# Kernel optimization log

Hardware: AMD Instinct MI355X
Metric: run time of the kernel (lower is better)

Reference implementation:

```python
import jax, jax.numpy as jnp
import numpy as np

N_NODES = 50000
N_EDGES = 800000
IN_C, HID_C, OUT_C = 128, 128, 64
BN_EPS = 1e-5


def _normalized_adj(edge_index, N):
    # Mirrors remove_self_loops + add_self_loops + symmetric GCN normalization.
    src, dst = edge_index[0], edge_index[1]
    mask = (src != dst).astype(jnp.float32)  # drop original self loops
    # degree of dst over (masked edges + added self loops)
    deg = jax.ops.segment_sum(mask, dst, num_segments=N) + 1.0
    dinv = jnp.where(deg > 0, deg ** -0.5, 0.0)
    w = mask * dinv[src] * dinv[dst]          # weights for original edges
    w_self = dinv * dinv                      # weights for added self loops
    return src, dst, w, w_self


def _spmm(src, dst, w, w_self, x):
    # torch.sparse.mm(adj, x): out[i] = sum_{e: src[e]=i} w[e] * x[dst[e]] + w_self[i]*x[i]
    agg = jax.ops.segment_sum(w[:, None] * x[dst], src, num_segments=x.shape[0])
    return agg + w_self[:, None] * x


def setup_inputs() -> dict:
    key = jax.random.key(0)
    ks = jax.random.split(key, 4)
    x = jax.random.normal(ks[0], (N_NODES, IN_C), dtype=jnp.float32)
    edge_index = jax.random.randint(ks[1], (2, N_EDGES), 0, N_NODES, dtype=jnp.int64)
    # glorot init for GCN linear weights
    s1 = np.sqrt(6.0 / (IN_C + HID_C)).astype(np.float32)
    s2 = np.sqrt(6.0 / (HID_C + OUT_C)).astype(np.float32)
    W1 = jax.random.uniform(ks[2], (IN_C, HID_C), jnp.float32, -s1, s1)
    W2 = jax.random.uniform(ks[3], (HID_C, OUT_C), jnp.float32, -s2, s2)
    return {
        "x": x,
        "edge_index": edge_index,
        "W1": W1,
        "b1": jnp.zeros((HID_C,), jnp.float32),
        "gamma": jnp.ones((HID_C,), jnp.float32),
        "beta": jnp.zeros((HID_C,), jnp.float32),
        "W2": W2,
        "b2": jnp.zeros((OUT_C,), jnp.float32),
    }


def reference(x, edge_index, W1, b1, gamma, beta, W2, b2):
    N = x.shape[0]
    src, dst, w, w_self = _normalized_adj(edge_index, N)
    # layer 1: linear -> SpMM -> BN (batch stats) -> ReLU (dropout: eval)
    h = x @ W1 + b1
    h = _spmm(src, dst, w, w_self, h)
    mean = h.mean(axis=0)
    var = jnp.mean((h - mean) ** 2, axis=0)
    h = (h - mean) * jax.lax.rsqrt(var + BN_EPS) * gamma + beta
    h = jax.nn.relu(h)
    # layer 2: linear -> SpMM
    h = h @ W2 + b2
    h = _spmm(src, dst, w, w_self, h)
    return h
```

## Files before the change

### kernel.cpp

```cpp
#include <hip/hip_runtime.h>

#define N_NODES 50000
#define N_EDGES 800000
#define BN_EPS 1e-5f
#define NPAD 50176
#define SCAN_BLOCKS 98

#define S_SLICES 64
#define R_RANGES 4
#define BINS 16384
#define NP4 (R_RANGES * BINS)
#define ES (N_EDGES / S_SLICES)

#define XS_STRIDE 68

typedef unsigned int uint;
typedef unsigned short ushort;
typedef float floatx4 __attribute__((ext_vector_type(4)));
typedef short bf16x8 __attribute__((ext_vector_type(8)));

__device__ __forceinline__ float bfl(uint u) { return __uint_as_float(u << 16); }
__device__ __forceinline__ float bfh(uint u) { return __uint_as_float(u & 0xffff0000u); }
__device__ __forceinline__ uint pack_bf2(float a, float b) {
    uint ua = __float_as_uint(a), ub = __float_as_uint(b);
    ua += 0x7fffu + ((ua >> 16) & 1u);
    ub += 0x7fffu + ((ub >> 16) & 1u);
    return (ua >> 16) | (ub & 0xffff0000u);
}
__device__ __forceinline__ ushort bf1(float x) {
    uint u = __float_as_uint(x);
    u += 0x7fffu + ((u >> 16) & 1u);
    return (ushort)(u >> 16);
}
__device__ __forceinline__ void acc8(float* a, uint4 h, float w) {
    a[0] += w * bfl(h.x); a[1] += w * bfh(h.x);
    a[2] += w * bfl(h.y); a[3] += w * bfh(h.y);
    a[4] += w * bfl(h.z); a[5] += w * bfh(h.z);
    a[6] += w * bfl(h.w); a[7] += w * bfh(h.w);
}

__global__ __launch_bounds__(256) void prep_w_kernel(const float* __restrict__ W1,
                                                     const float* __restrict__ W2,
                                                     uint* __restrict__ W1t,
                                                     uint* __restrict__ W2t) {
    int t = blockIdx.x * 256 + threadIdx.x;
    if (t < 8192) {
        int n = t >> 6, kk = t & 63;
        W1t[t] = pack_bf2(W1[(2 * kk) * 128 + n], W1[(2 * kk + 1) * 128 + n]);
    } else if (t < 12288) {
        int u = t - 8192;
        int n = u >> 6, kk = u & 63;
        W2t[u] = pack_bf2(W2[(2 * kk) * 64 + n], W2[(2 * kk + 1) * 64 + n]);
    }
}

__global__ __launch_bounds__(256) void count_hist_kernel(const int* __restrict__ src,
                                                         const int* __restrict__ dst,
                                                         ushort* __restrict__ part_cnt,
                                                         ushort* __restrict__ part_deg) {
    __shared__ uint cnt_lds[BINS / 2];
    __shared__ uint deg_lds[BINS / 2];
    const int s = blockIdx.x / R_RANGES;
    const int r = blockIdx.x % R_RANGES;
    const int base = r * BINS;
    for (int j = threadIdx.x; j < BINS / 2; j += 256) { cnt_lds[j] = 0u; deg_lds[j] = 0u; }
    __syncthreads();
    const int4* s4 = (const int4*)(src + s * ES);
    const int4* d4 = (const int4*)(dst + s * ES);
#pragma unroll 2
    for (int g = threadIdx.x; g < ES / 4; g += 256) {
        int4 sv = s4[g];
        int4 dv = d4[g];
#pragma unroll
        for (int k = 0; k < 4; ++k) {
            int ss = (&sv.x)[k], dd = (&dv.x)[k];
            if (ss != dd) {
                int a = ss - base;
                if ((unsigned)a < (unsigned)BINS)
                    atomicAdd(&cnt_lds[a >> 1], 1u << ((a & 1) * 16));
                int b = dd - base;
                if ((unsigned)b < (unsigned)BINS)
                    atomicAdd(&deg_lds[b >> 1], 1u << ((b & 1) * 16));
            }
        }
    }
    __syncthreads();
    uint* pc = (uint*)&part_cnt[s * NP4 + base];
    uint* pd = (uint*)&part_deg[s * NP4 + base];
    for (int j = threadIdx.x; j < BINS / 2; j += 256) { pc[j] = cnt_lds[j]; pd[j] = deg_lds[j]; }
}

__global__ __launch_bounds__(256) void dinv_rowcnt_kernel(const ushort* __restrict__ part_deg,
                                                          const ushort* __restrict__ part_cnt,
                                                          float* __restrict__ dinv,
                                                          int* __restrict__ rowcnt) {
    int i = (blockIdx.x * 256 + threadIdx.x) * 2;
    uint dg0 = 0, dg1 = 0, rc0 = 0, rc1 = 0;
#pragma unroll 8
    for (int s = 0; s < S_SLICES; ++s) {
        uint vd = *(const uint*)&part_deg[s * NP4 + i];
        uint vc = *(const uint*)&part_cnt[s * NP4 + i];
        dg0 += vd & 0xffffu; dg1 += vd >> 16;
        rc0 += vc & 0xffffu; rc1 += vc >> 16;
    }
    *(int2*)&rowcnt[i] = make_int2((int)rc0, (int)rc1);
    if (i < N_NODES) dinv[i] = rsqrtf((float)dg0 + 1.0f);
    if (i + 1 < N_NODES) dinv[i + 1] = rsqrtf((float)dg1 + 1.0f);
}

__global__ __launch_bounds__(512) void scan1_kernel(const int* __restrict__ rowcnt,
                                                    int* __restrict__ rowptr,
                                                    int* __restrict__ psum) {
    __shared__ int buf[512];
    int t = threadIdx.x;
    int g = blockIdx.x * 512 + t;
    buf[t] = rowcnt[g];
    __syncthreads();
#pragma unroll
    for (int off = 1; off < 512; off <<= 1) {
        int x = (t >= off) ? buf[t - off] : 0;
        __syncthreads();
        buf[t] += x;
        __syncthreads();
    }
    rowptr[g] = buf[t];
    if (t == 511) psum[blockIdx.x] = buf[511];
}

__global__ void scan2_kernel(int* __restrict__ psum) {
    if (threadIdx.x == 0) {
        int acc = 0;
        for (int i = 0; i < SCAN_BLOCKS; ++i) {
            int v = psum[i];
            psum[i] = acc;
            acc += v;
        }
    }
}

__global__ __launch_bounds__(256) void cursor_init_kernel(const int* __restrict__ rowcnt,
                                                          int* __restrict__ rowptr,
                                                          const int* __restrict__ psum,
                                                          const ushort* __restrict__ part_cnt,
                                                          int* __restrict__ cursor) {
    int i = (blockIdx.x * 256 + threadIdx.x) * 2;
    int ps = psum[i >> 9];
    int b0 = rowptr[i] - rowcnt[i] + ps;
    int b1 = rowptr[i + 1] - rowcnt[i + 1] + ps;
    *(int2*)&rowptr[i] = make_int2(b0, b1);
#pragma unroll 8
    for (int s = 0; s < S_SLICES; ++s) {
        *(int2*)&cursor[s * NP4 + i] = make_int2(b0, b1);
        uint vc = *(const uint*)&part_cnt[s * NP4 + i];
        b0 += (int)(vc & 0xffffu);
        b1 += (int)(vc >> 16);
    }
}

__global__ __launch_bounds__(256) void fill_lds_kernel(const int* __restrict__ src,
                                                       const int* __restrict__ dst,
                                                       const float* __restrict__ dinv,
                                                       const int* __restrict__ cursor,
                                                       int2* __restrict__ epair) {
    __shared__ int curs[BINS];
    const int s = blockIdx.x / R_RANGES;
    const int r = blockIdx.x % R_RANGES;
    const int base = r * BINS;
    const int* gc = &cursor[s * NP4 + base];
    for (int j = threadIdx.x; j < BINS; j += 256) curs[j] = gc[j];
    __syncthreads();
    const int4* s4 = (const int4*)(src + s * ES);
    const int4* d4 = (const int4*)(dst + s * ES);
#pragma unroll 2
    for (int g = threadIdx.x; g < ES / 4; g += 256) {
        int4 sv = s4[g];
        int4 dv = d4[g];
#pragma unroll
        for (int k = 0; k < 4; ++k) {
            int ss = (&sv.x)[k], dd = (&dv.x)[k];
            int a = ss - base;
            if (ss != dd && (unsigned)a < (unsigned)BINS) {
                int pos = atomicAdd(&curs[a], 1);
                epair[pos] = make_int2(dd, __float_as_int(dinv[ss] * dinv[dd]));
            }
        }
    }
}

__global__ __launch_bounds__(256) void gemm1_mfma_kernel(const float* __restrict__ X,
                                                         const uint* __restrict__ W1t,
                                                         const float* __restrict__ bias,
                                                         ushort* __restrict__ Hbf) {
    __shared__ uint lds[(64 + 128) * XS_STRIDE];
    uint* Xs = lds;
    uint* Ws = lds + 64 * XS_STRIDE;
    const int t = threadIdx.x;
    const int rowBase = blockIdx.x * 64;

    {
        int r = t >> 2, q = t & 3;
        int arow = rowBase + r;
        uint* xd = &Xs[r * XS_STRIDE + q * 16];
        if (arow < N_NODES) {
            const float4* xp = (const float4*)&X[arow * 128 + q * 32];
#pragma unroll
            for (int i = 0; i < 8; ++i) {
                float4 v = xp[i];
                xd[2 * i]     = pack_bf2(v.x, v.y);
                xd[2 * i + 1] = pack_bf2(v.z, v.w);
            }
        } else {
#pragma unroll
            for (int i = 0; i < 16; ++i) xd[i] = 0u;
        }
    }
    {
        int n = t >> 1, half = t & 1;
        const uint4* wp = (const uint4*)&W1t[n * 64 + half * 32];
        uint* wd = &Ws[n * XS_STRIDE + half * 32];
#pragma unroll
        for (int i = 0; i < 8; ++i) *(uint4*)&wd[i * 4] = wp[i];
    }
    __syncthreads();

    const int wv = t >> 6, lane = t & 63;
    const int lr = lane & 15;
    const int ko = (lane >> 4) * 4;
    const int m0 = wv * 16;
    floatx4 acc[8];
#pragma unroll
    for (int j = 0; j < 8; ++j) acc[j] = (floatx4){0.f, 0.f, 0.f, 0.f};

#pragma unroll
    for (int ks = 0; ks < 4; ++ks) {
        const int kb = ks * 16 + ko;
        bf16x8 a = *(bf16x8*)&Xs[(m0 + lr) * XS_STRIDE + kb];
#pragma unroll
        for (int j = 0; j < 8; ++j) {
            bf16x8 b = *(bf16x8*)&Ws[(j * 16 + lr) * XS_STRIDE + kb];
            acc[j] = __builtin_amdgcn_mfma_f32_16x16x32_bf16(a, b, acc[j], 0, 0, 0);
        }
    }
    const int rbase = rowBase + m0 + (lane >> 4) * 4;
#pragma unroll
    for (int j = 0; j < 8; ++j) {
        const int col = j * 16 + lr;
        const float bb = bias[col];
#pragma unroll
        for (int r = 0; r < 4; ++r) {
            int row = rbase + r;
            if (row < N_NODES) Hbf[row * 128 + col] = bf1(acc[j][r] + bb);
        }
    }
}

__global__ __launch_bounds__(256) void gemm2_mfma_kernel(const uint* __restrict__ Hin,
                                                         const uint* __restrict__ W2t,
                                                         const float* __restrict__ bias,
                                                         const float* __restrict__ scale,
                                                         const float* __restrict__ shift,
                                                         ushort* __restrict__ Hbf) {
    __shared__ uint lds[(64 + 64) * XS_STRIDE];
    uint* Xs = lds;
    uint* Ws = lds + 64 * XS_STRIDE;
    const int t = threadIdx.x;
    const int rowBase = blockIdx.x * 64;

    {
        int r = t >> 2, q = t & 3;
        int arow = rowBase + r;
        uint* xd = &Xs[r * XS_STRIDE + q * 16];
        if (arow < N_NODES) {
            const uint* hp = &Hin[arow * 64 + q * 16];
#pragma unroll
            for (int i = 0; i < 16; ++i) {
                uint u = hp[i];
                int m = q * 16 + i;
                float2 sc = *(const float2*)&scale[2 * m];
                float2 sh = *(const float2*)&shift[2 * m];
                float a0 = fmaxf(0.f, bfl(u) * sc.x + sh.x);
                float a1 = fmaxf(0.f, bfh(u) * sc.y + sh.y);
                xd[i] = pack_bf2(a0, a1);
            }
        } else {
#pragma unroll
            for (int i = 0; i < 16; ++i) xd[i] = 0u;
        }
    }
    if (t < 128) {
        int n = t >> 1, half = t & 1;
        const uint4* wp = (const uint4*)&W2t[n * 64 + half * 32];
        uint* wd = &Ws[n * XS_STRIDE + half * 32];
#pragma unroll
        for (int i = 0; i < 8; ++i) *(uint4*)&wd[i * 4] = wp[i];
    }
    __syncthreads();

    const int wv = t >> 6, lane = t & 63;
    const int lr = lane & 15;
    const int ko = (lane >> 4) * 4;
    const int m0 = wv * 16;
    floatx4 acc[4];
#pragma unroll
    for (int j = 0; j < 4; ++j) acc[j] = (floatx4){0.f, 0.f, 0.f, 0.f};

#pragma unroll
    for (int ks = 0; ks < 4; ++ks) {
        const int kb = ks * 16 + ko;
        bf16x8 a = *(bf16x8*)&Xs[(m0 + lr) * XS_STRIDE + kb];
#pragma unroll
        for (int j = 0; j < 4; ++j) {
            bf16x8 b = *(bf16x8*)&Ws[(j * 16 + lr) * XS_STRIDE + kb];
            acc[j] = __builtin_amdgcn_mfma_f32_16x16x32_bf16(a, b, acc[j], 0, 0, 0);
        }
    }
    const int rbase = rowBase + m0 + (lane >> 4) * 4;
#pragma unroll
    for (int j = 0; j < 4; ++j) {
        const int col = j * 16 + lr;
        const float bb = bias[col];
#pragma unroll
        for (int r = 0; r < 4; ++r) {
            int row = rbase + r;
            if (row < N_NODES) Hbf[row * 64 + col] = bf1(acc[j][r] + bb);
        }
    }
}

template <int C, bool OUT_BF16>
__global__ __launch_bounds__(256) void spmm_bf16_kernel(const int* __restrict__ rowptr,
                                                        const int2* __restrict__ epair,
                                                        const float* __restrict__ dinv,
                                                        const uint* __restrict__ H,
                                                        void* __restrict__ outv) {
    constexpr int LPR = C / 8;
    constexpr int RPB = 256 / LPR;
    constexpr int US  = C / 2;
    const int t = threadIdx.x;
    const int lane = t % LPR;
    const int row = blockIdx.x * RPB + t / LPR;
    if (row >= N_NODES) return;
    const int cu = lane * 4;
    const float di = dinv[row];

    float acc[8];
    {
        uint4 hv = *(const uint4*)&H[row * US + cu];
        float w = di * di;
        acc[0] = w * bfl(hv.x); acc[1] = w * bfh(hv.x);
        acc[2] = w * bfl(hv.y); acc[3] = w * bfh(hv.y);
        acc[4] = w * bfl(hv.z); acc[5] = w * bfh(hv.z);
        acc[6] = w * bfl(hv.w); acc[7] = w * bfh(hv.w);
    }
    const int e0 = rowptr[row], e1 = rowptr[row + 1];
    int e = e0;
    if ((e & 1) && e < e1) {
        int2 p = epair[e];
        uint4 h = *(const uint4*)&H[p.x * US + cu];
        acc8(acc, h, __int_as_float(p.y));
        ++e;
    }
    const int4* ep4 = (const int4*)epair;
    for (; e + 8 <= e1; e += 8) {
        int4 qa = ep4[(e >> 1) + 0];
        int4 qb = ep4[(e >> 1) + 1];
        int4 qc = ep4[(e >> 1) + 2];
        int4 qd = ep4[(e >> 1) + 3];
        uint4 h0 = *(const uint4*)&H[qa.x * US + cu];
        uint4 h1 = *(const uint4*)&H[qa.z * US + cu];
        uint4 h2 = *(const uint4*)&H[qb.x * US + cu];
        uint4 h3 = *(const uint4*)&H[qb.z * US + cu];
        uint4 h4 = *(const uint4*)&H[qc.x * US + cu];
        uint4 h5 = *(const uint4*)&H[qc.z * US + cu];
        uint4 h6 = *(const uint4*)&H[qd.x * US + cu];
        uint4 h7 = *(const uint4*)&H[qd.z * US + cu];
        acc8(acc, h0, __int_as_float(qa.y));
        acc8(acc, h1, __int_as_float(qa.w));
        acc8(acc, h2, __int_as_float(qb.y));
        acc8(acc, h3, __int_as_float(qb.w));
        acc8(acc, h4, __int_as_float(qc.y));
        acc8(acc, h5, __int_as_float(qc.w));
        acc8(acc, h6, __int_as_float(qd.y));
        acc8(acc, h7, __int_as_float(qd.w));
    }
    for (; e + 2 <= e1; e += 2) {
        int4 q = ep4[e >> 1];
        uint4 h0 = *(const uint4*)&H[q.x * US + cu];
        uint4 h1 = *(const uint4*)&H[q.z * US + cu];
        acc8(acc, h0, __int_as_float(q.y));
        acc8(acc, h1, __int_as_float(q.w));
    }
    if (e < e1) {
        int2 p = epair[e];
        uint4 h = *(const uint4*)&H[p.x * US + cu];
        acc8(acc, h, __int_as_float(p.y));
    }
    if (OUT_BF16) {
        uint4 o;
        o.x = pack_bf2(acc[0], acc[1]);
        o.y = pack_bf2(acc[2], acc[3]);
        o.z = pack_bf2(acc[4], acc[5]);
        o.w = pack_bf2(acc[6], acc[7]);
        *(uint4*)&((uint*)outv)[row * US + cu] = o;
    } else {
        float* out = (float*)outv;
        *(float4*)&out[row * C + lane * 8]     = make_float4(acc[0], acc[1], acc[2], acc[3]);
        *(float4*)&out[row * C + lane * 8 + 4] = make_float4(acc[4], acc[5], acc[6], acc[7]);
    }
}

__global__ __launch_bounds__(256) void bn_stats_kernel(const uint* __restrict__ H,
                                                       float* __restrict__ sum,
                                                       float* __restrict__ sumsq) {
    int uc = threadIdx.x & 63;
    int quarter = threadIdx.x >> 6;
    float s0 = 0.f, q0 = 0.f, s1 = 0.f, q1 = 0.f;
    for (int r = blockIdx.x * 4 + quarter; r < N_NODES; r += 512) {
        uint u = H[r * 64 + uc];
        float a = bfl(u), b = bfh(u);
        s0 += a; q0 += a * a;
        s1 += b; q1 += b * b;
    }
    __shared__ float red[4][256];
    red[0][threadIdx.x] = s0; red[1][threadIdx.x] = q0;
    red[2][threadIdx.x] = s1; red[3][threadIdx.x] = q1;
    __syncthreads();
    if (quarter == 0) {
        float ts0 = 0.f, tq0 = 0.f, ts1 = 0.f, tq1 = 0.f;
#pragma unroll
        for (int k = 0; k < 4; ++k) {
            ts0 += red[0][k * 64 + uc]; tq0 += red[1][k * 64 + uc];
            ts1 += red[2][k * 64 + uc]; tq1 += red[3][k * 64 + uc];
        }
        atomicAdd(&sum[2 * uc], ts0);
        atomicAdd(&sum[2 * uc + 1], ts1);
        atomicAdd(&sumsq[2 * uc], tq0);
        atomicAdd(&sumsq[2 * uc + 1], tq1);
    }
}

__global__ void bn_finalize_kernel(const float* __restrict__ sum,
                                   const float* __restrict__ sumsq,
                                   const float* __restrict__ gamma,
                                   const float* __restrict__ beta,
                                   float* __restrict__ scale,
                                   float* __restrict__ shift) {
    int c = threadIdx.x;
    if (c < 128) {
        float mean = sum[c] * (1.0f / N_NODES);
        float var = sumsq[c] * (1.0f / N_NODES) - mean * mean;
        float sc = gamma[c] * rsqrtf(var + BN_EPS);
        scale[c] = sc;
        shift[c] = beta[c] - mean * sc;
    }
}

extern "C" void kernel_launch(void* const* d_in, const int* in_sizes, int n_in,
                              void* d_out, int out_size, void* d_ws, size_t ws_size,
                              hipStream_t stream) {
    const float* x     = (const float*)d_in[0];
    const int*   ei    = (const int*)d_in[1];
    const float* W1    = (const float*)d_in[2];
    const float* b1    = (const float*)d_in[3];
    const float* gamma = (const float*)d_in[4];
    const float* beta  = (const float*)d_in[5];
    const float* W2    = (const float*)d_in[6];
    const float* b2    = (const float*)d_in[7];
    float* out = (float*)d_out;
    const int* src = ei;
    const int* dst = ei + N_EDGES;

    float* ws     = (float*)d_ws;
    float* dinv   = ws;
    float* stats  = ws + NPAD;
    int*   psum   = (int*)(ws + NPAD + 512);
    int*   rowcnt = psum + 128;
    int*   rowptr = rowcnt + NPAD;
    float* big    = (float*)(rowptr + NPAD);
    int2*   epair    = (int2*)big;
    ushort* part_cnt = (ushort*)(big + 1600000);
    ushort* part_deg = (ushort*)(big + 3700000);
    int*    cursor   = (int*)(big + 5800000);
    ushort* h1bf     = (ushort*)(big + 1600000);
    uint*   h1agg    = (uint*)(big + 4800000);
    ushort* h2bf     = h1bf;
    uint*   W1t      = (uint*)(big + 10000000);
    uint*   W2t      = W1t + 8192;
    float* sum    = stats;
    float* sumsq  = stats + 128;
    float* scale  = stats + 256;
    float* shift  = stats + 384;

    hipMemsetAsync(stats, 0, 512 * sizeof(float), stream);

    prep_w_kernel<<<48, 256, 0, stream>>>(W1, W2, W1t, W2t);

    count_hist_kernel<<<S_SLICES * R_RANGES, 256, 0, stream>>>(src, dst, part_cnt, part_deg);
    dinv_rowcnt_kernel<<<NPAD / 512, 256, 0, stream>>>(part_deg, part_cnt, dinv, rowcnt);

    scan1_kernel<<<SCAN_BLOCKS, 512, 0, stream>>>(rowcnt, rowptr, psum);
    scan2_kernel<<<1, 64, 0, stream>>>(psum);
    cursor_init_kernel<<<NPAD / 512, 256, 0, stream>>>(rowcnt, rowptr, psum, part_cnt, cursor);
    fill_lds_kernel<<<S_SLICES * R_RANGES, 256, 0, stream>>>(src, dst, dinv, cursor, epair);

    gemm1_mfma_kernel<<<(N_NODES + 63) / 64, 256, 0, stream>>>(x, W1t, b1, h1bf);

    spmm_bf16_kernel<128, true><<<(N_NODES + 15) / 16, 256, 0, stream>>>(
        rowptr, epair, dinv, (const uint*)h1bf, (void*)h1agg);

    bn_stats_kernel<<<128, 256, 0, stream>>>(h1agg, sum, sumsq);
    bn_finalize_kernel<<<1, 128, 0, stream>>>(sum, sumsq, gamma, beta, scale, shift);

    gemm2_mfma_kernel<<<(N_NODES + 63) / 64, 256, 0, stream>>>(h1agg, W2t, b2, scale, shift, h2bf);

    spmm_bf16_kernel<64, false><<<(N_NODES + 31) / 32, 256, 0, stream>>>(
        rowptr, epair, dinv, (const uint*)h2bf, (void*)out);
}
```

Measured before the change: 256.7 us.

## Fuse degree reduction with block scan and fold BN finalize into gemm2

Merges the degree/rowcount reduction with the per-block prefix scan, and moves the cross-block psum accumulation into cursor_init. The separate scan1, scan2 and bn_finalize launches and the memset go away. Stats zeroing now happens in the first block of the reduce kernel, and every gemm2 block computes BN scale and shift into shared memory. This removes several tiny serial launches and their gaps. In exchange it adds redundant per-block work in gemm2, a serial psum loop in thread 0 of each cursor_init block, and uses LDS-strided scale reads.

```diff
diff --git a/kernel.cpp b/kernel.cpp
--- a/kernel.cpp
+++ b/kernel.cpp
@@ -90,11 +90,16 @@
     for (int j = threadIdx.x; j < BINS / 2; j += 256) { pc[j] = cnt_lds[j]; pd[j] = deg_lds[j]; }
 }
 
-__global__ __launch_bounds__(256) void dinv_rowcnt_kernel(const ushort* __restrict__ part_deg,
+__global__ __launch_bounds__(256) void reduce_scan_kernel(const ushort* __restrict__ part_deg,
                                                           const ushort* __restrict__ part_cnt,
                                                           float* __restrict__ dinv,
-                                                          int* __restrict__ rowcnt) {
-    int i = (blockIdx.x * 256 + threadIdx.x) * 2;
+                                                          int* __restrict__ rowcnt,
+                                                          int* __restrict__ rowptr,
+                                                          int* __restrict__ psum,
+                                                          float* __restrict__ stats) {
+    const int t = threadIdx.x;
+    if (blockIdx.x == 0) stats[t] = 0.f;
+    const int i = blockIdx.x * 512 + 2 * t;
     uint dg0 = 0, dg1 = 0, rc0 = 0, rc1 = 0;
 #pragma unroll 8
     for (int s = 0; s < S_SLICES; ++s) {
@@ -106,36 +111,21 @@
     *(int2*)&rowcnt[i] = make_int2((int)rc0, (int)rc1);
     if (i < N_NODES) dinv[i] = rsqrtf((float)dg0 + 1.0f);
     if (i + 1 < N_NODES) dinv[i + 1] = rsqrtf((float)dg1 + 1.0f);
-}
-
-__global__ __launch_bounds__(512) void scan1_kernel(const int* __restrict__ rowcnt,
-                                                    int* __restrict__ rowptr,
-                                                    int* __restrict__ psum) {
-    __shared__ int buf[512];
-    int t = threadIdx.x;
-    int g = blockIdx.x * 512 + t;
-    buf[t] = rowcnt[g];
-    __syncthreads();
-#pragma unroll
-    for (int off = 1; off < 512; off <<= 1) {
-        int x = (t >= off) ? buf[t - off] : 0;
+
+    __shared__ int bs[256];
+    const int pair = (int)(rc0 + rc1);
+    bs[t] = pair;
+    __syncthreads();
+#pragma unroll
+    for (int off = 1; off < 256; off <<= 1) {
+        int x = (t >= off) ? bs[t - off] : 0;
         __syncthreads();
-        buf[t] += x;
+        bs[t] += x;
         __syncthreads();
     }
-    rowptr[g] = buf[t];
-    if (t == 511) psum[blockIdx.x] = buf[511];
-}
-
-__global__ void scan2_kernel(int* __restrict__ psum) {
-    if (threadIdx.x == 0) {
-        int acc = 0;
-        for (int i = 0; i < SCAN_BLOCKS; ++i) {
-            int v = psum[i];
-            psum[i] = acc;
-            acc += v;
-        }
-    }
+    const int excl = bs[t] - pair;
+    *(int2*)&rowptr[i] = make_int2(excl + (int)rc0, excl + pair);
+    if (t == 255) psum[blockIdx.x] = bs[255];
 }
 
 __global__ __launch_bounds__(256) void cursor_init_kernel(const int* __restrict__ rowcnt,
@@ -143,8 +133,19 @@
                                                           const int* __restrict__ psum,
                                                           const ushort* __restrict__ part_cnt,
                                                           int* __restrict__ cursor) {
-    int i = (blockIdx.x * 256 + threadIdx.x) * 2;
-    int ps = psum[i >> 9];
+    __shared__ int pbuf[SCAN_BLOCKS];
+    __shared__ int lps;
+    const int t = threadIdx.x;
+    if (t < SCAN_BLOCKS) pbuf[t] = psum[t];
+    __syncthreads();
+    if (t == 0) {
+        int acc = 0;
+        for (int j = 0; j < (int)blockIdx.x; ++j) acc += pbuf[j];
+        lps = acc;
+    }
+    __syncthreads();
+    const int ps = lps;
+    const int i = blockIdx.x * 512 + 2 * t;
     int b0 = rowptr[i] - rowcnt[i] + ps;
     int b1 = rowptr[i + 1] - rowcnt[i + 1] + ps;
     *(int2*)&rowptr[i] = make_int2(b0, b1);
@@ -257,14 +258,34 @@
 __global__ __launch_bounds__(256) void gemm2_mfma_kernel(const uint* __restrict__ Hin,
                                                          const uint* __restrict__ W2t,
                                                          const float* __restrict__ bias,
-                                                         const float* __restrict__ scale,
-                                                         const float* __restrict__ shift,
+                                                         const float* __restrict__ sum,
+                                                         const float* __restrict__ sumsq,
+                                                         const float* __restrict__ gamma,
+                                                         const float* __restrict__ beta,
                                                          ushort* __restrict__ Hbf) {
     __shared__ uint lds[(64 + 64) * XS_STRIDE];
+    __shared__ float sc_sh[128], sh_sh[128];
     uint* Xs = lds;
     uint* Ws = lds + 64 * XS_STRIDE;
     const int t = threadIdx.x;
     const int rowBase = blockIdx.x * 64;
+
+    if (t < 128) {
+        float mean = sum[t] * (1.0f / N_NODES);
+        float var = sumsq[t] * (1.0f / N_NODES) - mean * mean;
+        float sc = gamma[t] * rsqrtf(var + BN_EPS);
+        sc_sh[t] = sc;
+        sh_sh[t] = beta[t] - mean * sc;
+    }
+    if (t >= 128) {
+        int u = t - 128;
+        int n = u >> 1, half = u & 1;
+        const uint4* wp = (const uint4*)&W2t[n * 64 + half * 32];
+        uint* wd = &Ws[n * XS_STRIDE + half * 32];
+#pragma unroll
+        for (int i = 0; i < 8; ++i) *(uint4*)&wd[i * 4] = wp[i];
+    }
+    __syncthreads();
 
     {
         int r = t >> 2, q = t & 3;
@@ -276,23 +297,14 @@
             for (int i = 0; i < 16; ++i) {
                 uint u = hp[i];
                 int m = q * 16 + i;
-                float2 sc = *(const float2*)&scale[2 * m];
-                float2 sh = *(const float2*)&shift[2 * m];
-                float a0 = fmaxf(0.f, bfl(u) * sc.x + sh.x);
-                float a1 = fmaxf(0.f, bfh(u) * sc.y + sh.y);
+                float a0 = fmaxf(0.f, bfl(u) * sc_sh[2 * m] + sh_sh[2 * m]);
+                float a1 = fmaxf(0.f, bfh(u) * sc_sh[2 * m + 1] + sh_sh[2 * m + 1]);
                 xd[i] = pack_bf2(a0, a1);
             }
         } else {
 #pragma unroll
             for (int i = 0; i < 16; ++i) xd[i] = 0u;
         }
-    }
-    if (t < 128) {
-        int n = t >> 1, half = t & 1;
-        const uint4* wp = (const uint4*)&W2t[n * 64 + half * 32];
-        uint* wd = &Ws[n * XS_STRIDE + half * 32];
-#pragma unroll
-        for (int i = 0; i < 8; ++i) *(uint4*)&wd[i * 4] = wp[i];
     }
     __syncthreads();
 
@@ -439,22 +451,6 @@
     }
 }
 
-__global__ void bn_finalize_kernel(const float* __restrict__ sum,
-                                   const float* __restrict__ sumsq,
-                                   const float* __restrict__ gamma,
-                                   const float* __restrict__ beta,
-                                   float* __restrict__ scale,
-                                   float* __restrict__ shift) {
-    int c = threadIdx.x;
-    if (c < 128) {
-        float mean = sum[c] * (1.0f / N_NODES);
-        float var = sumsq[c] * (1.0f / N_NODES) - mean * mean;
-        float sc = gamma[c] * rsqrtf(var + BN_EPS);
-        scale[c] = sc;
-        shift[c] = beta[c] - mean * sc;
-    }
-}
-
 extern "C" void kernel_launch(void* const* d_in, const int* in_sizes, int n_in,
                               void* d_out, int out_size, void* d_ws, size_t ws_size,
                               hipStream_t stream) {
@@ -488,19 +484,13 @@
     uint*   W2t      = W1t + 8192;
     float* sum    = stats;
     float* sumsq  = stats + 128;
-    float* scale  = stats + 256;
-    float* shift  = stats + 384;
-
-    hipMemsetAsync(stats, 0, 512 * sizeof(float), stream);
 
     prep_w_kernel<<<48, 256, 0, stream>>>(W1, W2, W1t, W2t);
 
     count_hist_kernel<<<S_SLICES * R_RANGES, 256, 0, stream>>>(src, dst, part_cnt, part_deg);
-    dinv_rowcnt_kernel<<<NPAD / 512, 256, 0, stream>>>(part_deg, part_cnt, dinv, rowcnt);
-
-    scan1_kernel<<<SCAN_BLOCKS, 512, 0, stream>>>(rowcnt, rowptr, psum);
-    scan2_kernel<<<1, 64, 0, stream>>>(psum);
-    cursor_init_kernel<<<NPAD / 512, 256, 0, stream>>>(rowcnt, rowptr, psum, part_cnt, cursor);
+    reduce_scan_kernel<<<SCAN_BLOCKS, 256, 0, stream>>>(part_deg, part_cnt, dinv, rowcnt,
+                                                        rowptr, psum, stats);
+    cursor_init_kernel<<<SCAN_BLOCKS, 256, 0, stream>>>(rowcnt, rowptr, psum, part_cnt, cursor);
     fill_lds_kernel<<<S_SLICES * R_RANGES, 256, 0, stream>>>(src, dst, dinv, cursor, epair);
 
     gemm1_mfma_kernel<<<(N_NODES + 63) / 64, 256, 0, stream>>>(x, W1t, b1, h1bf);
@@ -509,9 +499,9 @@
         rowptr, epair, dinv, (const uint*)h1bf, (void*)h1agg);
 
     bn_stats_kernel<<<128, 256, 0, stream>>>(h1agg, sum, sumsq);
-    bn_finalize_kernel<<<1, 128, 0, stream>>>(sum, sumsq, gamma, beta, scale, shift);
-
-    gemm2_mfma_kernel<<<(N_NODES + 63) / 64, 256, 0, stream>>>(h1agg, W2t, b2, scale, shift, h2bf);
+
+    gemm2_mfma_kernel<<<(N_NODES + 63) / 64, 256, 0, stream>>>(h1agg, W2t, b2, sum, sumsq,
+                                                               gamma, beta, h2bf);
 
     spmm_bf16_kernel<64, false><<<(N_NODES + 31) / 32, 256, 0, stream>>>(
         rowptr, epair, dinv, (const uint*)h2bf, (void*)out);
```

Result: faster. 245.8 us (-4.2%).
